# Optimization experiments

Hardware: AMD Instinct MI355X
Metric: run time of the kernel (lower is better)

The kernel has to match this reference:

```python
import jax, jax.numpy as jnp
import numpy as np

N, E = 50000, 800000
IN, HID, H, OUT = 128, 32, 4, 40
K_SAMPLE, EPS_K = 25.0, 1e-3  # fixed k=25 (no dp_budget), compute_beta eps


def _glorot(key, shape):
    fan_in, fan_out = shape[0], shape[-1]
    lim = jnp.sqrt(6.0 / (fan_in + fan_out))
    return jax.random.uniform(key, shape, jnp.float32, -lim, lim)


def setup_inputs() -> dict:
    key = jax.random.key(0)
    ks = jax.random.split(key, 16)
    x = jax.random.normal(ks[0], (N, IN), jnp.float32)
    edge_index = jax.random.randint(ks[1], (2, E), 0, N, jnp.int64)
    # layer 0: IN -> (H, HID)
    W0 = _glorot(ks[2], (IN, H * HID)); as0 = _glorot(ks[3], (H, HID)); ad0 = _glorot(ks[4], (H, HID)); b0 = jnp.zeros((H * HID,), jnp.float32)
    # layer 1: H*HID -> (H, HID)
    W1 = _glorot(ks[5], (H * HID, H * HID)); as1 = _glorot(ks[6], (H, HID)); ad1 = _glorot(ks[7], (H, HID)); b1 = jnp.zeros((H * HID,), jnp.float32)
    # layer 2: H*HID -> (1, OUT)
    W2 = _glorot(ks[8], (H * HID, OUT)); as2 = _glorot(ks[9], (1, OUT)); ad2 = _glorot(ks[10], (1, OUT)); b2 = jnp.zeros((OUT,), jnp.float32)
    # BatchNorm affine params (batch-stat mode, deterministic)
    g_bn0 = jnp.ones((H * HID,), jnp.float32); be_bn0 = jnp.zeros((H * HID,), jnp.float32)
    g_bn1 = jnp.ones((H * HID,), jnp.float32); be_bn1 = jnp.zeros((H * HID,), jnp.float32)
    return {"x": x, "edge_index": edge_index,
            "W0": W0, "as0": as0, "ad0": ad0, "b0": b0,
            "W1": W1, "as1": as1, "ad1": ad1, "b1": b1,
            "W2": W2, "as2": as2, "ad2": ad2, "b2": b2,
            "g_bn0": g_bn0, "be_bn0": be_bn0, "g_bn1": g_bn1, "be_bn1": be_bn1}


def gat_conv(x, src, dst, W, a_src, a_dst, bias, heads, d_out):
    # PyG GATConv, add_self_loops=False, concat over heads
    h = (x @ W).reshape(-1, heads, d_out)                       # [N,H,D]
    al_s = jnp.sum(h * a_src, axis=-1)                          # [N,H]
    al_d = jnp.sum(h * a_dst, axis=-1)                          # [N,H]
    e = jax.nn.leaky_relu(al_s[src] + al_d[dst], 0.2)           # [E,H]
    m = jax.ops.segment_max(e, dst, num_segments=N)
    m = jnp.where(jnp.isfinite(m), m, 0.0)                      # guard empty segments
    p = jnp.exp(e - m[dst])
    s = jax.ops.segment_sum(p, dst, num_segments=N)
    alpha = p / (s[dst] + 1e-16)                                # segment softmax over incoming edges
    out = jax.ops.segment_sum(alpha[:, :, None] * h[src], dst, num_segments=N)  # [N,H,D]
    return out.reshape(-1, heads * d_out) + bias


def batch_norm(x, gamma, beta):
    mu = jnp.mean(x, axis=0)
    var = jnp.mean(jnp.square(x - mu), axis=0)
    return gamma * (x - mu) * jax.lax.rsqrt(var + 1e-5) + beta


def beta_scale(l):
    return 1.0 + 1.0 / (l + 1.0) * (1.0 / (K_SAMPLE + EPS_K))


def reference(x, edge_index, W0, as0, ad0, b0, W1, as1, ad1, b1, W2, as2, ad2, b2,
              g_bn0, be_bn0, g_bn1, be_bn1):
    src, dst = edge_index[0], edge_index[1]
    h = gat_conv(x, src, dst, W0, as0, ad0, b0, H, HID)
    h = jax.nn.elu(batch_norm(h, g_bn0, be_bn0)) * beta_scale(0)
    h = gat_conv(h, src, dst, W1, as1, ad1, b1, H, HID)
    h = jax.nn.elu(batch_norm(h, g_bn1, be_bn1)) * beta_scale(1)
    h = gat_conv(h, src, dst, W2, as2, ad2, b2, 1, OUT)
    return jax.nn.log_softmax(h, axis=1)
```

## Files before the change

kernel.cpp:

```cpp
#include <hip/hip_runtime.h>
#include <math.h>

#define N_NODES 50000
#define N_EDGES 800000
#define DIN 128
#define DHID 128
#define NH 4
#define HID 32
#define DOUT 40

#define PB 128
#define NPB 391

typedef __fp16 fp16x2 __attribute__((ext_vector_type(2)));
using s16x8 = __attribute__((ext_vector_type(8))) short;
using f32x4v = __attribute__((ext_vector_type(4))) float;

static __device__ __forceinline__ float lrelu(float x) { return x > 0.f ? x : 0.2f * x; }

static __device__ __forceinline__ unsigned int pkh(float a, float b) {
    union { fp16x2 h2; unsigned int u; } cv;
    cv.h2 = __builtin_amdgcn_cvt_pkrtz(a, b);
    return cv.u;
}
static __device__ __forceinline__ unsigned short f2h(float a) {
    union { _Float16 h; unsigned short s; } cv;
    cv.h = (_Float16)a;
    return cv.s;
}
static __device__ __forceinline__ unsigned short f2bf(float f) {
    unsigned int u = __float_as_uint(f);
    u = (u + 0x7FFFu + ((u >> 16) & 1u)) >> 16;
    return (unsigned short)u;
}

static __device__ __forceinline__ void fma8(float* acc, uint4 w, float p) {
    union { unsigned int u; _Float16 h[2]; } c0, c1, c2, c3;
    c0.u = w.x; c1.u = w.y; c2.u = w.z; c3.u = w.w;
    acc[0] = fmaf((float)c0.h[0], p, acc[0]);
    acc[1] = fmaf((float)c0.h[1], p, acc[1]);
    acc[2] = fmaf((float)c1.h[0], p, acc[2]);
    acc[3] = fmaf((float)c1.h[1], p, acc[3]);
    acc[4] = fmaf((float)c2.h[0], p, acc[4]);
    acc[5] = fmaf((float)c2.h[1], p, acc[5]);
    acc[6] = fmaf((float)c3.h[0], p, acc[6]);
    acc[7] = fmaf((float)c3.h[1], p, acc[7]);
}

static __device__ __forceinline__ float4 bnelu4(float4 x, float4 sc, float4 sh, float bs) {
    float y0 = fmaf(x.x, sc.x, sh.x);
    float y1 = fmaf(x.y, sc.y, sh.y);
    float y2 = fmaf(x.z, sc.z, sh.z);
    float y3 = fmaf(x.w, sc.w, sh.w);
    y0 = (y0 > 0.f ? y0 : __expf(y0) - 1.f) * bs;
    y1 = (y1 > 0.f ? y1 : __expf(y1) - 1.f) * bs;
    y2 = (y2 > 0.f ? y2 : __expf(y2) - 1.f) * bs;
    y3 = (y3 > 0.f ? y3 : __expf(y3) - 1.f) * bs;
    return {y0, y1, y2, y3};
}

__global__ __launch_bounds__(256) void bucket_hist_kernel(const int* __restrict__ dstv, int* __restrict__ bhist) {
    __shared__ int h[PB];
    if (threadIdx.x < PB) h[threadIdx.x] = 0;
    __syncthreads();
    for (int i = blockIdx.x * blockDim.x + threadIdx.x; i < N_EDGES; i += gridDim.x * blockDim.x)
        atomicAdd(&h[(unsigned)dstv[i] / NPB], 1);
    __syncthreads();
    if (threadIdx.x < PB) atomicAdd(&bhist[threadIdx.x], h[threadIdx.x]);
}

__global__ __launch_bounds__(128) void bucket_scan_kernel(const int* __restrict__ bhist,
                                                          int* __restrict__ bucket_base, int* __restrict__ cursor) {
    __shared__ int sA[PB], sB[PB];
    int t = threadIdx.x;
    sA[t] = bhist[t];
    __syncthreads();
    int* s = sA; int* d2 = sB;
    for (int off = 1; off < PB; off <<= 1) {
        d2[t] = s[t] + (t >= off ? s[t - off] : 0);
        __syncthreads();
        int* tmp = s; s = d2; d2 = tmp;
    }
    int excl = s[t] - bhist[t];
    bucket_base[t] = excl;
    cursor[t] = excl;
    if (t == PB - 1) bucket_base[PB] = s[t];
}

__global__ __launch_bounds__(256) void partition_kernel(const int* __restrict__ srcv, const int* __restrict__ dstv,
                                                        int* __restrict__ cursor, unsigned* __restrict__ part) {
    __shared__ unsigned rec[2048];
    __shared__ int cnt[PB], lofs[PB], gbase[PB];
    __shared__ int sA[PB], sB[PB];
    __shared__ int tot_s;
    const int t = threadIdx.x;
    const int base0 = blockIdx.x * 4096;
    for (int round = 0; round < 2; ++round) {
        int rbase = base0 + round * 2048;
        if (t < PB) cnt[t] = 0;
        __syncthreads();
        int myb[8]; int myr[8]; unsigned myrec[8];
#pragma unroll
        for (int i = 0; i < 8; ++i) {
            int e = rbase + i * 256 + t;
            bool valid = e < N_EDGES;
            int sv = valid ? srcv[e] : 0;
            int dv = valid ? dstv[e] : 0;
            myrec[i] = ((unsigned)sv << 16) | (unsigned)dv;
            int b = (unsigned)dv / NPB;
            myb[i] = valid ? b : -1;
            myr[i] = valid ? atomicAdd(&cnt[b], 1) : 0;
        }
        __syncthreads();
        if (t < PB) sA[t] = cnt[t];
        __syncthreads();
        int* s = sA; int* d2 = sB;
        for (int off = 1; off < PB; off <<= 1) {
            if (t < PB) d2[t] = s[t] + (t >= off ? s[t - off] : 0);
            __syncthreads();
            int* tmp = s; s = d2; d2 = tmp;
        }
        if (t < PB) {
            int c = cnt[t];
            lofs[t] = s[t] - c;
            gbase[t] = c > 0 ? atomicAdd(&cursor[t], c) : 0;
            if (t == PB - 1) tot_s = s[t];
        }
        __syncthreads();
#pragma unroll
        for (int i = 0; i < 8; ++i)
            if (myb[i] >= 0) rec[lofs[myb[i]] + myr[i]] = myrec[i];
        __syncthreads();
        int tot = tot_s;
#pragma unroll
        for (int i = 0; i < 8; ++i) {
            int lp = i * 256 + t;
            if (lp < tot) {
                unsigned r = rec[lp];
                int b = (r & 0xFFFFu) / NPB;
                part[gbase[b] + (lp - lofs[b])] = r;
            }
        }
        __syncthreads();
    }
}

__global__ __launch_bounds__(256) void bucket_csr_kernel(const unsigned* __restrict__ part, const int* __restrict__ bucket_base,
                                                         int* __restrict__ row_ptr, int* __restrict__ csr_src) {
    __shared__ int hist[512], sA[512], sB[512], cur[NPB];
    const int b = blockIdx.x, t = threadIdx.x;
    const int base = bucket_base[b];
    const int n = bucket_base[b + 1] - base;
    hist[t] = 0; hist[t + 256] = 0;
    __syncthreads();
    for (int i = t; i < n; i += 256)
        atomicAdd(&hist[(part[base + i] & 0xFFFFu) - b * NPB], 1);
    __syncthreads();
    sA[t] = hist[t]; sA[t + 256] = hist[t + 256];
    __syncthreads();
    int* s = sA; int* d2 = sB;
    for (int off = 1; off < 512; off <<= 1) {
        d2[t] = s[t] + (t >= off ? s[t - off] : 0);
        int u = t + 256;
        d2[u] = s[u] + (u >= off ? s[u - off] : 0);
        __syncthreads();
        int* tmp = s; s = d2; d2 = tmp;
    }
    for (int j = t; j < NPB; j += 256) {
        int node = b * NPB + j;
        int excl = s[j] - hist[j];
        if (node < N_NODES) row_ptr[node] = base + excl;
        cur[j] = excl;
    }
    if (b == PB - 1 && t == 0) row_ptr[N_NODES] = N_EDGES;
    __syncthreads();
    for (int i = t; i < n; i += 256) {
        unsigned r = part[base + i];
        int loc = (int)(r & 0xFFFFu) - b * NPB;
        int p = atomicAdd(&cur[loc], 1);
        csr_src[base + p] = (int)(r >> 16);
    }
}

__global__ __launch_bounds__(256) void gemm128_kernel(
    const float* __restrict__ X, const float* __restrict__ W,
    const float* __restrict__ a_src, const float* __restrict__ a_dst,
    const float* __restrict__ sums, const float* __restrict__ sqs,
    const float* __restrict__ gamma, const float* __restrict__ beta, float bscale, int apply_bn,
    unsigned short* __restrict__ Hout16, float* __restrict__ als, float* __restrict__ ald) {
    __shared__ unsigned int Xl[64][68];
    __shared__ unsigned short Wf[16384];
    __shared__ float scale_s[DHID], shift_s[DHID];
    const int t = threadIdx.x;
    const int w = t >> 6, l = t & 63;
    const int r0 = blockIdx.x * 64;

    if (apply_bn && t < DHID) {
        float mu = sums[t] * (1.f / N_NODES);
        float var = sqs[t] * (1.f / N_NODES) - mu * mu;
        float sc = gamma[t] * rsqrtf(var + 1e-5f);
        scale_s[t] = sc;
        shift_s[t] = beta[t] - mu * sc;
    }
    __syncthreads();

    {
        int sr = t >> 2, sa = t & 3;
        int gr = r0 + sr; gr = gr < N_NODES ? gr : N_NODES - 1;
        const float* Xrow = X + (size_t)gr * 128;
#pragma unroll
        for (int q = 0; q < 4; ++q) {
            int k0 = q * 32 + sa * 8;
            float4 xa = *(const float4*)(Xrow + k0);
            float4 xb = *(const float4*)(Xrow + k0 + 4);
            if (apply_bn) {
                xa = bnelu4(xa, *(const float4*)(scale_s + k0), *(const float4*)(shift_s + k0), bscale);
                xb = bnelu4(xb, *(const float4*)(scale_s + k0 + 4), *(const float4*)(shift_s + k0 + 4), bscale);
            }
            unsigned int* dst = &Xl[sr][k0 >> 1];
            dst[0] = (unsigned)f2bf(xa.x) | ((unsigned)f2bf(xa.y) << 16);
            dst[1] = (unsigned)f2bf(xa.z) | ((unsigned)f2bf(xa.w) << 16);
            dst[2] = (unsigned)f2bf(xb.x) | ((unsigned)f2bf(xb.y) << 16);
            dst[3] = (unsigned)f2bf(xb.z) | ((unsigned)f2bf(xb.w) << 16);
        }
    }
#pragma unroll 4
    for (int i = 0; i < 64; ++i) {
        int idx = i * 256 + t;
        int k = idx >> 7, c = idx & 127;
        float wv = W[idx];
        int ks = k >> 5, kr = k & 31;
        int lfrag = ((kr >> 3) << 4) | (c & 15);
        int slot = lfrag ^ ((lfrag >> 3) & 3);
        Wf[(((ks << 3) + (c >> 4)) * 64 + slot) * 8 + (kr & 7)] = f2bf(wv);
    }
    __syncthreads();

    f32x4v acc[8];
#pragma unroll
    for (int ct = 0; ct < 8; ++ct) acc[ct] = {0.f, 0.f, 0.f, 0.f};
    const int cl = l & 15, g = l >> 4;
    const int slotR = l ^ ((l >> 3) & 3);
    const unsigned short* XrowL = (const unsigned short*)&Xl[16 * w + cl][0];
#pragma unroll
    for (int ks = 0; ks < 4; ++ks) {
        s16x8 afrag = *(const s16x8*)(XrowL + ks * 32 + g * 8);
#pragma unroll
        for (int ct = 0; ct < 8; ++ct) {
            s16x8 bfrag = *(const s16x8*)&Wf[(((ks << 3) + ct) * 64 + slotR) * 8];
            acc[ct] = __builtin_amdgcn_mfma_f32_16x16x32_bf16(afrag, bfrag, acc[ct], 0, 0, 0);
        }
    }

    float asv[8], adv[8];
#pragma unroll
    for (int ct = 0; ct < 8; ++ct) {
        asv[ct] = a_src[ct * 16 + cl];
        adv[ct] = a_dst[ct * 16 + cl];
    }
#pragma unroll
    for (int r = 0; r < 4; ++r) {
        int node = r0 + 16 * w + 4 * g + r;
        bool valid = node < N_NODES;
        if (valid) {
#pragma unroll
            for (int ct = 0; ct < 8; ++ct)
                Hout16[(size_t)node * 128 + ct * 16 + cl] = f2h(acc[ct][r]);
        }
        float ps[4], pd[4];
#pragma unroll
        for (int h = 0; h < 4; ++h) {
            ps[h] = acc[2 * h][r] * asv[2 * h] + acc[2 * h + 1][r] * asv[2 * h + 1];
            pd[h] = acc[2 * h][r] * adv[2 * h] + acc[2 * h + 1][r] * adv[2 * h + 1];
#pragma unroll
            for (int off = 1; off < 16; off <<= 1) {
                ps[h] += __shfl_xor(ps[h], off);
                pd[h] += __shfl_xor(pd[h], off);
            }
        }
        if (valid && cl == 0) {
#pragma unroll
            for (int h = 0; h < 4; ++h) {
                als[node * 4 + h] = ps[h];
                ald[node * 4 + h] = pd[h];
            }
        }
    }
}

__global__ __launch_bounds__(256) void gemm40_kernel(
    const float* __restrict__ X, const float* __restrict__ W,
    const float* __restrict__ a_src, const float* __restrict__ a_dst,
    const float* __restrict__ sums, const float* __restrict__ sqs,
    const float* __restrict__ gamma, const float* __restrict__ beta, float bscale,
    unsigned short* __restrict__ Hout, float* __restrict__ als, float* __restrict__ ald) {
    __shared__ float Xs[64][36];
    __shared__ float Ws[40][36];
    __shared__ float scale_s[DHID], shift_s[DHID];
    const int t = threadIdx.x;
    const int tx = t & 7, ty = t >> 3;
    const int r0 = blockIdx.x * 64;
    const int sr = t >> 2, sa = t & 3;

    if (t < DHID) {
        float mu = sums[t] * (1.f / N_NODES);
        float var = sqs[t] * (1.f / N_NODES) - mu * mu;
        float sc = gamma[t] * rsqrtf(var + 1e-5f);
        scale_s[t] = sc;
        shift_s[t] = beta[t] - mu * sc;
    }
    __syncthreads();

    int gr = r0 + sr; gr = gr < N_NODES ? gr : N_NODES - 1;
    const float* Xrow = X + (size_t)gr * 128;
    float4 xpreA = bnelu4(*(const float4*)(Xrow + 8 * sa),
                          *(const float4*)(scale_s + 8 * sa), *(const float4*)(shift_s + 8 * sa), bscale);
    float4 xpreB = bnelu4(*(const float4*)(Xrow + 8 * sa + 4),
                          *(const float4*)(scale_s + 8 * sa + 4), *(const float4*)(shift_s + 8 * sa + 4), bscale);
    float wpre[5];
#pragma unroll
    for (int i = 0; i < 5; ++i) wpre[i] = W[t + 256 * i];

    float acc[2][5];
#pragma unroll
    for (int i = 0; i < 2; ++i)
#pragma unroll
        for (int j = 0; j < 5; ++j) acc[i][j] = 0.f;

    for (int step = 0; step < 4; ++step) {
        __syncthreads();
        *(float4*)&Xs[sr][8 * sa] = xpreA;
        *(float4*)&Xs[sr][8 * sa + 4] = xpreB;
#pragma unroll
        for (int i = 0; i < 5; ++i) {
            int idx = t + 256 * i;
            Ws[idx % 40][idx / 40] = wpre[i];
        }
        if (step < 3) {
            int k0 = (step + 1) * 32;
            xpreA = bnelu4(*(const float4*)(Xrow + k0 + 8 * sa),
                           *(const float4*)(scale_s + k0 + 8 * sa), *(const float4*)(shift_s + k0 + 8 * sa), bscale);
            xpreB = bnelu4(*(const float4*)(Xrow + k0 + 8 * sa + 4),
                           *(const float4*)(scale_s + k0 + 8 * sa + 4), *(const float4*)(shift_s + k0 + 8 * sa + 4), bscale);
#pragma unroll
            for (int i = 0; i < 5; ++i) wpre[i] = W[k0 * 40 + t + 256 * i];
        }
        __syncthreads();
#pragma unroll
        for (int kk4 = 0; kk4 < 8; ++kk4) {
            float4 xa = *(const float4*)&Xs[2 * ty][4 * kk4];
            float4 xb = *(const float4*)&Xs[2 * ty + 1][4 * kk4];
#pragma unroll
            for (int j = 0; j < 5; ++j) {
                float4 wv = *(const float4*)&Ws[tx + 8 * j][4 * kk4];
                acc[0][j] = fmaf(xa.x, wv.x, acc[0][j]);
                acc[0][j] = fmaf(xa.y, wv.y, acc[0][j]);
                acc[0][j] = fmaf(xa.z, wv.z, acc[0][j]);
                acc[0][j] = fmaf(xa.w, wv.w, acc[0][j]);
                acc[1][j] = fmaf(xb.x, wv.x, acc[1][j]);
                acc[1][j] = fmaf(xb.y, wv.y, acc[1][j]);
                acc[1][j] = fmaf(xb.z, wv.z, acc[1][j]);
                acc[1][j] = fmaf(xb.w, wv.w, acc[1][j]);
            }
        }
    }
    float asv[5], adv[5];
#pragma unroll
    for (int j = 0; j < 5; ++j) {
        asv[j] = a_src[tx + 8 * j];
        adv[j] = a_dst[tx + 8 * j];
    }
#pragma unroll
    for (int i = 0; i < 2; ++i) {
        int r = r0 + 2 * ty + i;
        bool valid = r < N_NODES;
        if (valid) {
#pragma unroll
            for (int j = 0; j < 5; ++j)
                Hout[(size_t)r * 40 + tx + 8 * j] = f2h(acc[i][j]);
        }
        float ps = 0.f, pd = 0.f;
#pragma unroll
        for (int j = 0; j < 5; ++j) {
            ps = fmaf(acc[i][j], asv[j], ps);
            pd = fmaf(acc[i][j], adv[j], pd);
        }
#pragma unroll
        for (int off = 1; off < 8; off <<= 1) {
            ps += __shfl_xor(ps, off);
            pd += __shfl_xor(pd, off);
        }
        if (valid && tx == 0) {
            als[r] = ps;
            ald[r] = pd;
        }
    }
}

__global__ __launch_bounds__(256) void agg128_kernel(
    const int* __restrict__ row_ptr, const int* __restrict__ csr_src,
    const unsigned int* __restrict__ Ht, const float* __restrict__ als, const float* __restrict__ ald,
    const float* __restrict__ bias, float* __restrict__ out) {
    __shared__ float s_p[4][256];
    __shared__ int s_u[4][64];
    int v = (blockIdx.x * blockDim.x + threadIdx.x) >> 6;
    v = __builtin_amdgcn_readfirstlane(v);
    int lane = threadIdx.x & 63;
    int wslot = threadIdx.x >> 6;
    if (v >= N_NODES) return;
    int beg = row_ptr[v], end = row_ptr[v + 1];
    float4 ad4 = *(const float4*)(ald + (size_t)v * 4);
    const int g = lane >> 4;
    const int li = lane & 15;
    const int hh = li >> 2;
    float tsum = 0.f;
    float acc[8];
#pragma unroll
    for (int j = 0; j < 8; ++j) acc[j] = 0.f;

    for (int cbeg = beg; cbeg < end; cbeg += 64) {
        int cnt = min(64, end - cbeg);
        bool act = lane < cnt;
        int u = act ? csr_src[cbeg + lane] : 0;
        float p0, p1, p2, p3;
        if (act) {
            float4 s4 = *(const float4*)(als + (size_t)u * 4);
            p0 = __expf(lrelu(s4.x + ad4.x));
            p1 = __expf(lrelu(s4.y + ad4.y));
            p2 = __expf(lrelu(s4.z + ad4.z));
            p3 = __expf(lrelu(s4.w + ad4.w));
        } else {
            p0 = p1 = p2 = p3 = 0.f;
        }
        s_u[wslot][lane] = u;
        float4 pv = {p0, p1, p2, p3};
        *(float4*)&s_p[wslot][lane * 4] = pv;
        for (int i = 0; i < cnt; i += 8) {
            int ea = i + g;
            int eb = i + 4 + g;
            int ua = s_u[wslot][ea];
            int ub = s_u[wslot][eb];
            float pa = s_p[wslot][ea * 4 + hh];
            float pb = s_p[wslot][eb * 4 + hh];
            uint4 wa = *(const uint4*)(Ht + (size_t)ua * 64 + li * 4);
            uint4 wb = *(const uint4*)(Ht + (size_t)ub * 64 + li * 4);
            tsum += pa + pb;
            fma8(acc, wa, pa);
            fma8(acc, wb, pb);
        }
    }
#pragma unroll
    for (int j = 0; j < 8; ++j) {
        acc[j] += __shfl_xor(acc[j], 16);
        acc[j] += __shfl_xor(acc[j], 32);
    }
    tsum += __shfl_xor(tsum, 16);
    tsum += __shfl_xor(tsum, 32);
    float inv = 1.f / (tsum + 1e-16f);
    if (g == 0) {
        float4 b0 = *(const float4*)(bias + 8 * li);
        float4 b1 = *(const float4*)(bias + 8 * li + 4);
        float4 o0 = {acc[0] * inv + b0.x, acc[1] * inv + b0.y, acc[2] * inv + b0.z, acc[3] * inv + b0.w};
        float4 o1 = {acc[4] * inv + b1.x, acc[5] * inv + b1.y, acc[6] * inv + b1.z, acc[7] * inv + b1.w};
        *(float4*)(out + (size_t)v * DHID + 8 * li) = o0;
        *(float4*)(out + (size_t)v * DHID + 8 * li + 4) = o1;
    }
}

__global__ __launch_bounds__(256) void agg40_kernel(
    const int* __restrict__ row_ptr, const int* __restrict__ csr_src,
    const uint4* __restrict__ Ht4, const float* __restrict__ als, const float* __restrict__ ald,
    const float* __restrict__ bias, float* __restrict__ out) {
    __shared__ float s_p[4][76];
    __shared__ int s_u[4][76];
    __shared__ float s_red[4][12][41];
    int v = (blockIdx.x * blockDim.x + threadIdx.x) >> 6;
    v = __builtin_amdgcn_readfirstlane(v);
    int lane = threadIdx.x & 63;
    int wslot = threadIdx.x >> 6;
    if (v >= N_NODES) return;
    int beg = row_ptr[v], end = row_ptr[v + 1];
    float adv = ald[v];
    const int g = lane / 5;
    const int li = lane - g * 5;
    const bool gact = lane < 60;
    if (lane < 12) { s_u[wslot][64 + lane] = 0; s_p[wslot][64 + lane] = 0.f; }
    float tsum = 0.f;
    float a[8];
#pragma unroll
    for (int j = 0; j < 8; ++j) a[j] = 0.f;

    for (int cbeg = beg; cbeg < end; cbeg += 64) {
        int cnt = min(64, end - cbeg);
        bool act = lane < cnt;
        int u = act ? csr_src[cbeg + lane] : 0;
        float p = act ? __expf(lrelu(als[u] + adv)) : 0.f;
        s_u[wslot][lane] = u;
        s_p[wslot][lane] = p;
        for (int i = 0; i < cnt; i += 12) {
            int e = i + g;
            int uu = s_u[wslot][e];
            float pp = s_p[wslot][e];
            uint4 w = {0u, 0u, 0u, 0u};
            if (gact) w = Ht4[(size_t)uu * 5 + li];
            if (gact) tsum += pp;
            fma8(a, w, pp);
        }
    }
    if (gact) {
#pragma unroll
        for (int j = 0; j < 8; ++j) s_red[wslot][g][li * 8 + j] = a[j];
        if (li == 0) s_red[wslot][g][40] = tsum;
    }
    bool fown = lane < DOUT;
    float accf = 0.f, T = 0.f;
#pragma unroll
    for (int g2 = 0; g2 < 12; ++g2) {
        if (fown) accf += s_red[wslot][g2][lane];
        T += s_red[wslot][g2][40];
    }
    float inv = 1.f / (T + 1e-16f);
    float z = fown ? (accf * inv + bias[lane]) : -1e30f;
    float zm = z;
#pragma unroll
    for (int off = 1; off < 64; off <<= 1) zm = fmaxf(zm, __shfl_xor(zm, off));
    float se = fown ? __expf(z - zm) : 0.f;
#pragma unroll
    for (int off = 1; off < 64; off <<= 1) se += __shfl_xor(se, off);
    float ls = zm + logf(se);
    if (fown) out[(size_t)v * DOUT + lane] = z - ls;
}

__global__ __launch_bounds__(256) void bn_stats_kernel(const float* __restrict__ X,
                                                       float* __restrict__ sums, float* __restrict__ sqs) {
    const int t = threadIdx.x;
    const int tid = blockIdx.x * 256 + t;
    const float4* X4 = (const float4*)X;
    float4 s = {0.f, 0.f, 0.f, 0.f}, q = {0.f, 0.f, 0.f, 0.f};
    for (int i = tid; i < N_NODES * 32; i += 500 * 256) {
        float4 vv = X4[i];
        s.x += vv.x; s.y += vv.y; s.z += vv.z; s.w += vv.w;
        q.x += vv.x * vv.x; q.y += vv.y * vv.y; q.z += vv.z * vv.z; q.w += vv.w * vv.w;
    }
    __shared__ float ls[1024], lq[1024];
    *(float4*)&ls[t * 4] = s;
    *(float4*)&lq[t * 4] = q;
    __syncthreads();
    if (t < 128) {
        int c4 = t >> 2, j = t & 3;
        float S = 0.f, Q = 0.f;
#pragma unroll
        for (int k = 0; k < 8; ++k) {
            S += ls[(c4 + 32 * k) * 4 + j];
            Q += lq[(c4 + 32 * k) * 4 + j];
        }
        atomicAdd(&sums[t], S);
        atomicAdd(&sqs[t], Q);
    }
}

extern "C" void kernel_launch(void* const* d_in, const int* in_sizes, int n_in,
                              void* d_out, int out_size, void* d_ws, size_t ws_size,
                              hipStream_t stream) {
    (void)in_sizes; (void)n_in; (void)out_size; (void)ws_size;
    const float* x = (const float*)d_in[0];
    const int* ei = (const int*)d_in[1];
    const float* W0 = (const float*)d_in[2];
    const float* as0 = (const float*)d_in[3];
    const float* ad0 = (const float*)d_in[4];
    const float* b0 = (const float*)d_in[5];
    const float* W1 = (const float*)d_in[6];
    const float* as1 = (const float*)d_in[7];
    const float* ad1 = (const float*)d_in[8];
    const float* b1 = (const float*)d_in[9];
    const float* W2 = (const float*)d_in[10];
    const float* as2 = (const float*)d_in[11];
    const float* ad2 = (const float*)d_in[12];
    const float* b2 = (const float*)d_in[13];
    const float* g_bn0 = (const float*)d_in[14];
    const float* be_bn0 = (const float*)d_in[15];
    const float* g_bn1 = (const float*)d_in[16];
    const float* be_bn1 = (const float*)d_in[17];
    float* out = (float*)d_out;

    const int* srcv = ei;
    const int* dstv = ei + N_EDGES;

    char* p = (char*)d_ws;
    auto carve = [&](size_t bytes) {
        char* q = p;
        p += (bytes + 255) & ~(size_t)255;
        return q;
    };
    unsigned int* h_bf = (unsigned int*)carve((size_t)N_NODES * 64 * 4);
    float* agg   = (float*)carve((size_t)N_NODES * DHID * 4);
    float* als   = (float*)carve((size_t)N_NODES * NH * 4);
    float* ald   = (float*)carve((size_t)N_NODES * NH * 4);
    int* row_ptr = (int*)carve((size_t)(N_NODES + 1) * 4);
    int* csr_src = (int*)carve((size_t)N_EDGES * 4);
    unsigned* part = (unsigned*)carve((size_t)N_EDGES * 4);
    int* bhist   = (int*)carve((PB + 512) * 4);
    float* sums0 = (float*)(bhist + PB);
    float* sqs0  = sums0 + 128;
    float* sums1 = sqs0 + 128;
    float* sqs1  = sums1 + 128;
    int* bucket_base = (int*)carve((PB + 1) * 4);
    int* cursor  = (int*)carve(PB * 4);

    const float bs0 = 1.0f + 1.0f / 25.001f;
    const float bs1 = 1.0f + 0.5f / 25.001f;

    const int RT64 = (N_NODES + 63) / 64;
    const int G128B = RT64;
    const int G40B = RT64;
    const int AB = (N_NODES * 64 + 255) / 256;
    const int PARTB = (N_EDGES + 4095) / 4096;

    hipMemsetAsync(bhist, 0, (PB + 512) * 4, stream);
    bucket_hist_kernel<<<400, 256, 0, stream>>>(dstv, bhist);
    bucket_scan_kernel<<<1, PB, 0, stream>>>(bhist, bucket_base, cursor);
    partition_kernel<<<PARTB, 256, 0, stream>>>(srcv, dstv, cursor, part);
    bucket_csr_kernel<<<PB, 256, 0, stream>>>(part, bucket_base, row_ptr, csr_src);

    gemm128_kernel<<<G128B, 256, 0, stream>>>(x, W0, as0, ad0, nullptr, nullptr, nullptr, nullptr, 1.f, 0,
                                              (unsigned short*)h_bf, als, ald);
    agg128_kernel<<<AB, 256, 0, stream>>>(row_ptr, csr_src, h_bf, als, ald, b0, agg);
    bn_stats_kernel<<<500, 256, 0, stream>>>(agg, sums0, sqs0);

    gemm128_kernel<<<G128B, 256, 0, stream>>>(agg, W1, as1, ad1, sums0, sqs0, g_bn0, be_bn0, bs0, 1,
                                              (unsigned short*)h_bf, als, ald);
    agg128_kernel<<<AB, 256, 0, stream>>>(row_ptr, csr_src, h_bf, als, ald, b1, agg);
    bn_stats_kernel<<<500, 256, 0, stream>>>(agg, sums1, sqs1);

    gemm40_kernel<<<G40B, 256, 0, stream>>>(agg, W2, as2, ad2, sums1, sqs1, g_bn1, be_bn1, bs1, (unsigned short*)h_bf, als, ald);
    agg40_kernel<<<AB, 256, 0, stream>>>(row_ptr, csr_src, (const uint4*)h_bf, als, ald, b2, out);
}
```

Measured before the change: 248.9 us.

## Map one 16-lane group per node in agg128 instead of one wave per node

The 128-wide aggregation kernel now gives each node its own 16-lane group, so each wave handles four nodes. Before, a whole 64-lane wave served one node and split its edges across four groups. The change drops the cross-group shuffle reduction and the mostly idle 64-lane edge-chunk loads, since the average degree is about 16. In exchange, the four nodes in a wave can have different in-degrees, so the loop runs as long as the longest one and lanes can diverge. The grid size for agg128 is adjusted to match, and an unused helper replaces the removed pkh function.

```diff
diff --git a/kernel.cpp b/kernel.cpp
--- a/kernel.cpp
+++ b/kernel.cpp
@@ -18,11 +18,12 @@
 
 static __device__ __forceinline__ float lrelu(float x) { return x > 0.f ? x : 0.2f * x; }
 
-static __device__ __forceinline__ unsigned int pkh(float a, float b) {
-    union { fp16x2 h2; unsigned int u; } cv;
-    cv.h2 = __builtin_amdgcn_cvt_pkrtz(a, b);
-    return cv.u;
-}
+static __device__ __forceinline__ float sel4(int h, float a, float b, float c, float d) {
+    float ab = (h & 1) ? b : a;
+    float cd = (h & 1) ? d : c;
+    return (h & 2) ? cd : ab;
+}
+
 static __device__ __forceinline__ unsigned short f2h(float a) {
     union { _Float16 h; unsigned short s; } cv;
     cv.h = (_Float16)a;
@@ -399,29 +400,31 @@
 
 __global__ __launch_bounds__(256) void agg128_kernel(
     const int* __restrict__ row_ptr, const int* __restrict__ csr_src,
-    const unsigned int* __restrict__ Ht, const float* __restrict__ als, const float* __restrict__ ald,
+    const uint4* __restrict__ Ht4, const float* __restrict__ als, const float* __restrict__ ald,
     const float* __restrict__ bias, float* __restrict__ out) {
-    __shared__ float s_p[4][256];
-    __shared__ int s_u[4][64];
-    int v = (blockIdx.x * blockDim.x + threadIdx.x) >> 6;
-    v = __builtin_amdgcn_readfirstlane(v);
-    int lane = threadIdx.x & 63;
-    int wslot = threadIdx.x >> 6;
-    if (v >= N_NODES) return;
+    __shared__ int s_u[16][17];
+    __shared__ float s_p[16][68];
+    const int t = threadIdx.x;
+    const int lane = t & 63;
+    const int wslot = t >> 6;
+    const int g = lane >> 4, li = lane & 15;
+    const int slot = wslot * 4 + g;
+    const int wid = (blockIdx.x * 256 + t) >> 6;
+    const int vraw = wid * 4 + g;
+    const bool vvalid = vraw < N_NODES;
+    const int v = vvalid ? vraw : N_NODES - 1;
+    const int hh = li >> 2;
     int beg = row_ptr[v], end = row_ptr[v + 1];
     float4 ad4 = *(const float4*)(ald + (size_t)v * 4);
-    const int g = lane >> 4;
-    const int li = lane & 15;
-    const int hh = li >> 2;
     float tsum = 0.f;
     float acc[8];
 #pragma unroll
     for (int j = 0; j < 8; ++j) acc[j] = 0.f;
 
-    for (int cbeg = beg; cbeg < end; cbeg += 64) {
-        int cnt = min(64, end - cbeg);
-        bool act = lane < cnt;
-        int u = act ? csr_src[cbeg + lane] : 0;
+    for (int cbeg = beg; cbeg < end; cbeg += 16) {
+        int cnt = min(16, end - cbeg);
+        bool act = li < cnt;
+        int u = act ? csr_src[cbeg + li] : 0;
         float p0, p1, p2, p3;
         if (act) {
             float4 s4 = *(const float4*)(als + (size_t)u * 4);
@@ -432,32 +435,23 @@
         } else {
             p0 = p1 = p2 = p3 = 0.f;
         }
-        s_u[wslot][lane] = u;
+        s_u[slot][li] = u;
         float4 pv = {p0, p1, p2, p3};
-        *(float4*)&s_p[wslot][lane * 4] = pv;
-        for (int i = 0; i < cnt; i += 8) {
-            int ea = i + g;
-            int eb = i + 4 + g;
-            int ua = s_u[wslot][ea];
-            int ub = s_u[wslot][eb];
-            float pa = s_p[wslot][ea * 4 + hh];
-            float pb = s_p[wslot][eb * 4 + hh];
-            uint4 wa = *(const uint4*)(Ht + (size_t)ua * 64 + li * 4);
-            uint4 wb = *(const uint4*)(Ht + (size_t)ub * 64 + li * 4);
+        *(float4*)&s_p[slot][li * 4] = pv;
+        for (int i = 0; i < cnt; i += 2) {
+            int u0 = s_u[slot][i];
+            int u1 = s_u[slot][i + 1];
+            float pa = s_p[slot][i * 4 + hh];
+            float pb = s_p[slot][(i + 1) * 4 + hh];
+            uint4 wa = Ht4[(size_t)u0 * 16 + li];
+            uint4 wb = Ht4[(size_t)u1 * 16 + li];
             tsum += pa + pb;
             fma8(acc, wa, pa);
             fma8(acc, wb, pb);
         }
     }
-#pragma unroll
-    for (int j = 0; j < 8; ++j) {
-        acc[j] += __shfl_xor(acc[j], 16);
-        acc[j] += __shfl_xor(acc[j], 32);
-    }
-    tsum += __shfl_xor(tsum, 16);
-    tsum += __shfl_xor(tsum, 32);
     float inv = 1.f / (tsum + 1e-16f);
-    if (g == 0) {
+    if (vvalid) {
         float4 b0 = *(const float4*)(bias + 8 * li);
         float4 b1 = *(const float4*)(bias + 8 * li + 4);
         float4 o0 = {acc[0] * inv + b0.x, acc[1] * inv + b0.y, acc[2] * inv + b0.z, acc[3] * inv + b0.w};
@@ -613,7 +607,8 @@
     const int RT64 = (N_NODES + 63) / 64;
     const int G128B = RT64;
     const int G40B = RT64;
-    const int AB = (N_NODES * 64 + 255) / 256;
+    const int A128B = (N_NODES + 15) / 16;
+    const int A40B = (N_NODES * 64 + 255) / 256;
     const int PARTB = (N_EDGES + 4095) / 4096;
 
     hipMemsetAsync(bhist, 0, (PB + 512) * 4, stream);
@@ -624,14 +619,14 @@
 
     gemm128_kernel<<<G128B, 256, 0, stream>>>(x, W0, as0, ad0, nullptr, nullptr, nullptr, nullptr, 1.f, 0,
                                               (unsigned short*)h_bf, als, ald);
-    agg128_kernel<<<AB, 256, 0, stream>>>(row_ptr, csr_src, h_bf, als, ald, b0, agg);
+    agg128_kernel<<<A128B, 256, 0, stream>>>(row_ptr, csr_src, (const uint4*)h_bf, als, ald, b0, agg);
     bn_stats_kernel<<<500, 256, 0, stream>>>(agg, sums0, sqs0);
 
     gemm128_kernel<<<G128B, 256, 0, stream>>>(agg, W1, as1, ad1, sums0, sqs0, g_bn0, be_bn0, bs0, 1,
                                               (unsigned short*)h_bf, als, ald);
-    agg128_kernel<<<AB, 256, 0, stream>>>(row_ptr, csr_src, h_bf, als, ald, b1, agg);
+    agg128_kernel<<<A128B, 256, 0, stream>>>(row_ptr, csr_src, (const uint4*)h_bf, als, ald, b1, agg);
     bn_stats_kernel<<<500, 256, 0, stream>>>(agg, sums1, sqs1);
 
     gemm40_kernel<<<G40B, 256, 0, stream>>>(agg, W2, as2, ad2, sums1, sqs1, g_bn1, be_bn1, bs1, (unsigned short*)h_bf, als, ald);
-    agg40_kernel<<<AB, 256, 0, stream>>>(row_ptr, csr_src, (const uint4*)h_bf, als, ald, b2, out);
-}
+    agg40_kernel<<<A40B, 256, 0, stream>>>(row_ptr, csr_src, (const uint4*)h_bf, als, ald, b2, out);
+}
```

After: 249.9 us. No clear change (+0.4%).
